# Kernel optimization log

Measured on AMD Instinct MI355X. Metric: run time of the kernel, lower is better.

The kernel has to match this reference:

```python
import jax, jax.numpy as jnp
import numpy as np


def setup_inputs() -> dict:
    key = jax.random.key(0)
    ks = jax.random.split(key, 5)
    Bsz, T, d = 8, 2048, 1024
    x = jax.random.normal(ks[0], (Bsz, T, d), dtype=jnp.float32)
    W_in = jax.random.normal(ks[1], (d, d), dtype=jnp.float32) * (1.0 / np.sqrt(d))
    b_in = jnp.zeros((d,), dtype=jnp.float32)
    log_A = -jnp.ones((d,), dtype=jnp.float32)  # keras Constant(-1.0) init
    B_vec = jax.random.normal(ks[2], (d,), dtype=jnp.float32) * 0.05  # keras random_normal stddev
    C = jax.random.normal(ks[3], (d, d), dtype=jnp.float32) * 0.05
    D = jnp.zeros((d,), dtype=jnp.float32)
    return {"x": x, "W_in": W_in, "b_in": b_in, "log_A": log_A, "B_vec": B_vec, "C": C, "D": D}


def reference(x, W_in, b_in, log_A, B_vec, C, D):
    # u = in_proj(x)
    u = jnp.einsum('btd,de->bte', x, W_in) + b_in            # [B,T,d]
    A = -jnp.exp(log_A)                                       # [d]
    # linear recurrence h_t = h_{t-1} * A + u_t * B, h_0 = 0
    # expressed as an associative scan over pairs (a_t, b_t):
    #   (a1,b1) o (a2,b2) = (a1*a2, b1*a2 + b2)
    b = u * B_vec                                             # [B,T,d]
    a = jnp.broadcast_to(A, b.shape)                          # [B,T,d]

    def combine(e1, e2):
        a1, b1 = e1
        a2, b2 = e2
        return (a1 * a2, b1 * a2 + b2)

    _, h_seq = jax.lax.associative_scan(combine, (a, b), axis=1)  # h_t, [B,T,d]
    y = jnp.einsum('bts,sd->btd', h_seq, C)
    return y + x * D
```

## Files before the change

kernel.cpp:

```cpp
#include <hip/hip_runtime.h>
#include <hip/hip_bf16.h>

typedef unsigned short ushort_t;
typedef __bf16 bf16x8 __attribute__((ext_vector_type(8)));
typedef float f32x4 __attribute__((ext_vector_type(4)));

#define BM 128
#define BN 128
#define BK 64

__device__ __forceinline__ float bf2f(ushort_t u) {
    union { unsigned int i; float f; } x; x.i = ((unsigned int)u) << 16; return x.f;
}
__device__ __forceinline__ ushort_t f2bf(float f) {
    __hip_bfloat16 h = __float2bfloat16(f);
    return *(ushort_t*)&h;
}
__device__ __forceinline__ void async16(const void* g, void* l) {
    __builtin_amdgcn_global_load_lds((const __attribute__((address_space(1))) void*)g,
                                     (__attribute__((address_space(3))) void*)l, 16, 0, 0);
}

__global__ void prep_fused(const float* __restrict__ x, const float* __restrict__ W_in,
                           const float* __restrict__ C, const float* __restrict__ Bv,
                           __hip_bfloat16* __restrict__ xb, __hip_bfloat16* __restrict__ Wpt,
                           __hip_bfloat16* __restrict__ Ct) {
    int bid = blockIdx.x;
    if (bid < 16384) {
        size_t idx = ((size_t)bid * 256 + threadIdx.x) * 4;
        float4 v = *(const float4*)(x + idx);
        ushort4 ov;
        ov.x = f2bf(v.x); ov.y = f2bf(v.y); ov.z = f2bf(v.z); ov.w = f2bf(v.w);
        *(ushort4*)((ushort_t*)xb + idx) = ov;
        return;
    }
    __shared__ float tile[32][33];
    const float* in;
    __hip_bfloat16* out;
    bool do_scale;
    int lid;
    if (bid < 17408) { lid = bid - 16384; in = W_in; out = Wpt; do_scale = true; }
    else             { lid = bid - 17408; in = C;    out = Ct;  do_scale = false; }
    int bx = (lid & 31) * 32;
    int by = (lid >> 5) * 32;
    int tx = threadIdx.x & 31, ty = threadIdx.x >> 5;
    #pragma unroll
    for (int i = 0; i < 32; i += 8)
        tile[ty + i][tx] = in[(size_t)(by + ty + i) * 1024 + bx + tx];
    __syncthreads();
    if (threadIdx.x < 128) {
        int n_local = threadIdx.x & 31;
        int quad    = threadIdx.x >> 5;
        int n = bx + n_local;
        float s = do_scale ? Bv[n] : 1.0f;
        int lr     = n & 15;
        int n_tile = n >> 4;
        int k_tile = by >> 5;
        ushort_t buf[8];
        #pragma unroll
        for (int j = 0; j < 8; ++j)
            buf[j] = f2bf(tile[quad * 8 + j][n_local] * s);
        size_t off = (((size_t)n_tile * 32 + k_tile) * 64 + quad * 16 + lr) * 8;
        ushort_t* dst = (ushort_t*)out + off;
        *(ushort4*)dst       = *(ushort4*)&buf[0];
        *(ushort4*)(dst + 4) = *(ushort4*)&buf[4];
    }
}

template <int EPI>
__global__ __launch_bounds__(256) void gemm_bt(
    const __hip_bfloat16* __restrict__ Ab, const __hip_bfloat16* __restrict__ Bpk,
    int M, int N, int K,
    const float* __restrict__ b_in, const float* __restrict__ Bv,
    __hip_bfloat16* __restrict__ out_bf,
    const __hip_bfloat16* __restrict__ xres_bf, const float* __restrict__ Dvec,
    float* __restrict__ out_f) {
    const int tid  = threadIdx.x;
    const int wave = tid >> 6;
    const int lane = tid & 63;
    const int quad = lane >> 4;
    const int lr   = lane & 15;
    const int wm   = wave >> 1;
    const int wn   = wave & 1;

    const int lin   = blockIdx.y * gridDim.x + blockIdx.x;
    const int xcd   = lin & 7;
    const int local = lin >> 3;
    const int m_blk = xcd * 16 + (local >> 3);
    const int n_blk = local & 7;
    const int m0 = m_blk * BM;
    const int n0 = n_blk * BN;

    __shared__ __align__(16) ushort_t sA[BM * BK];

    const ushort_t* A  = (const ushort_t*)Ab;
    const ushort_t* Bp = (const ushort_t*)Bpk;
    const int ktiles = K >> 5;
    const int ntile0 = n0 >> 4;

    f32x4 acc[4][4];
    #pragma unroll
    for (int i = 0; i < 4; ++i)
        #pragma unroll
        for (int j = 0; j < 4; ++j)
            #pragma unroll
            for (int r = 0; r < 4; ++r) acc[i][j][r] = 0.0f;

    const int row8 = lane >> 3;
    const int schunk = (lane & 7) ^ row8;
    const int ldcol = schunk * 8;
    for (int k0 = 0; k0 < K; k0 += BK) {
        __syncthreads();
        #pragma unroll
        for (int j = 0; j < 4; ++j) {
            int c = j * 4 + wave;
            int row = c * 8 + row8;
            const ushort_t* gA = A + (size_t)(m0 + row) * K + k0 + ldcol;
            async16(gA, &sA[c * 512]);
        }
        __syncthreads();
        #pragma unroll
        for (int kk = 0; kk < BK; kk += 32) {
            const int kt = (k0 + kk) >> 5;
            bf16x8 bfr[4];
            #pragma unroll
            for (int j = 0; j < 4; ++j)
                bfr[j] = *(const bf16x8*)&Bp[((((size_t)(ntile0 + wn * 4 + j)) * ktiles + kt) * 64 + lane) * 8];
            const int ck = (kk >> 3) + quad;
            const int pc = (ck ^ (lr & 7)) * 8;
            bf16x8 af[4];
            #pragma unroll
            for (int i = 0; i < 4; ++i)
                af[i] = *(const bf16x8*)&sA[(wm * 64 + i * 16 + lr) * BK + pc];
            #pragma unroll
            for (int i = 0; i < 4; ++i)
                #pragma unroll
                for (int j = 0; j < 4; ++j)
                    acc[i][j] = __builtin_amdgcn_mfma_f32_16x16x32_bf16(af[i], bfr[j], acc[i][j], 0, 0, 0);
        }
    }

    if constexpr (EPI == 0) {
        ushort_t* st = sA;
        #pragma unroll
        for (int i = 0; i < 4; ++i) {
            __syncthreads();
            #pragma unroll
            for (int j = 0; j < 4; ++j) {
                int colL = wn * 64 + j * 16 + lr;
                float bs = b_in[n0 + colL] * Bv[n0 + colL];
                #pragma unroll
                for (int r = 0; r < 4; ++r) {
                    int r32 = wm * 16 + quad * 4 + r;
                    st[r32 * 136 + colL] = f2bf(acc[i][j][r] + bs);
                }
            }
            __syncthreads();
            int r32 = tid >> 3;
            int cch = (tid & 7) * 16;
            int row_g = m0 + (r32 >> 4) * 64 + i * 16 + (r32 & 15);
            bf16x8 v0 = *(const bf16x8*)&st[r32 * 136 + cch];
            bf16x8 v1 = *(const bf16x8*)&st[r32 * 136 + cch + 8];
            ushort_t* dst = (ushort_t*)out_bf + (size_t)row_g * N + n0 + cch;
            *(bf16x8*)dst       = v0;
            *(bf16x8*)(dst + 8) = v1;
        }
    } else {
        #pragma unroll
        for (int i = 0; i < 4; ++i) {
            int row = m0 + wm * 64 + i * 16 + quad * 4;
            #pragma unroll
            for (int j = 0; j < 4; ++j) {
                int col = n0 + wn * 64 + j * 16 + lr;
                float dv = Dvec[col];
                #pragma unroll
                for (int r = 0; r < 4; ++r) {
                    float xv = bf2f(((const ushort_t*)xres_bf)[(size_t)(row + r) * N + col]);
                    out_f[(size_t)(row + r) * N + col] = acc[i][j][r] + xv * dv;
                }
            }
        }
    }
}

#define SCH 32
__global__ void scan_kernel(const __hip_bfloat16* __restrict__ b, __hip_bfloat16* __restrict__ h,
                            const float* __restrict__ logA, int T, int DD) {
    int c0 = (blockIdx.z * 256 + threadIdx.x) * 2;
    int q  = blockIdx.x;
    int bb = blockIdx.y;
    float2 la = *(const float2*)(logA + c0);
    float a0 = -__expf(la.x), a1 = -__expf(la.y);
    float a0_2 = a0 * a0,   a1_2 = a1 * a1;
    float a0_3 = a0_2 * a0, a1_3 = a1_2 * a1;
    float a0_4 = a0_2 * a0_2, a1_4 = a1_2 * a1_2;
    int ts = q * SCH;
    size_t base = (size_t)bb * T * DD + c0;
    float h0 = 0.f, h1 = 0.f;
    if (ts > 0) {
        const ushort_t* wp = (const ushort_t*)b + base + (size_t)(ts - 32) * DD;
        #pragma unroll
        for (int t = 0; t < 32; t += 4) {
            ushort2 v0 = *(const ushort2*)(wp);
            ushort2 v1 = *(const ushort2*)(wp + DD);
            ushort2 v2 = *(const ushort2*)(wp + 2 * (size_t)DD);
            ushort2 v3 = *(const ushort2*)(wp + 3 * (size_t)DD);
            wp += 4 * (size_t)DD;
            float s0 = fmaf(a0_3, bf2f(v0.x), fmaf(a0_2, bf2f(v1.x), fmaf(a0, bf2f(v2.x), bf2f(v3.x))));
            float s1 = fmaf(a1_3, bf2f(v0.y), fmaf(a1_2, bf2f(v1.y), fmaf(a1, bf2f(v2.y), bf2f(v3.y))));
            h0 = fmaf(a0_4, h0, s0);
            h1 = fmaf(a1_4, h1, s1);
        }
    }
    const ushort_t* bp = (const ushort_t*)b + base + (size_t)ts * DD;
    ushort_t* hp = (ushort_t*)h + base + (size_t)ts * DD;
    #pragma unroll
    for (int t = 0; t < SCH; t += 4) {
        ushort2 v0 = *(const ushort2*)(bp);
        ushort2 v1 = *(const ushort2*)(bp + DD);
        ushort2 v2 = *(const ushort2*)(bp + 2 * (size_t)DD);
        ushort2 v3 = *(const ushort2*)(bp + 3 * (size_t)DD);
        bp += 4 * (size_t)DD;
        ushort2 o;
        h0 = fmaf(a0, h0, bf2f(v0.x)); h1 = fmaf(a1, h1, bf2f(v0.y));
        o.x = f2bf(h0); o.y = f2bf(h1); *(ushort2*)hp = o;
        h0 = fmaf(a0, h0, bf2f(v1.x)); h1 = fmaf(a1, h1, bf2f(v1.y));
        o.x = f2bf(h0); o.y = f2bf(h1); *(ushort2*)(hp + DD) = o;
        h0 = fmaf(a0, h0, bf2f(v2.x)); h1 = fmaf(a1, h1, bf2f(v2.y));
        o.x = f2bf(h0); o.y = f2bf(h1); *(ushort2*)(hp + 2 * (size_t)DD) = o;
        h0 = fmaf(a0, h0, bf2f(v3.x)); h1 = fmaf(a1, h1, bf2f(v3.y));
        o.x = f2bf(h0); o.y = f2bf(h1); *(ushort2*)(hp + 3 * (size_t)DD) = o;
        hp += 4 * (size_t)DD;
    }
}

extern "C" void kernel_launch(void* const* d_in, const int* in_sizes, int n_in,
                              void* d_out, int out_size, void* d_ws, size_t ws_size,
                              hipStream_t stream) {
    const float* x    = (const float*)d_in[0];
    const float* W_in = (const float*)d_in[1];
    const float* b_in = (const float*)d_in[2];
    const float* logA = (const float*)d_in[3];
    const float* Bv   = (const float*)d_in[4];
    const float* C    = (const float*)d_in[5];
    const float* Dv   = (const float*)d_in[6];
    float* out = (float*)d_out;

    const int Bsz = 8, T = 2048, d = 1024;
    const int M = Bsz * T;

    char* w = (char*)d_ws;
    __hip_bfloat16* xb   = (__hip_bfloat16*)w;
    __hip_bfloat16* Wpt  = xb + (size_t)M * d;
    __hip_bfloat16* Ct   = Wpt + (size_t)d * d;
    __hip_bfloat16* bbuf = Ct + (size_t)d * d;
    __hip_bfloat16* hbuf = bbuf + (size_t)M * d;

    prep_fused<<<16384 + 2048, 256, 0, stream>>>(x, W_in, C, Bv, xb, Wpt, Ct);

    gemm_bt<0><<<dim3(d / BN, M / BM), 256, 0, stream>>>(
        xb, Wpt, M, d, d, b_in, Bv, bbuf, nullptr, nullptr, nullptr);
    scan_kernel<<<dim3(T / SCH, Bsz, 2), 256, 0, stream>>>(bbuf, hbuf, logA, T, d);
    gemm_bt<1><<<dim3(d / BN, M / BM), 256, 0, stream>>>(
        hbuf, Ct, M, d, d, nullptr, nullptr, nullptr, xb, Dv, out);
}
```

Baseline: 245.9 us.

## Fuse fp32-to-bf16 conversion of x into GEMM load path and retune scan chunking

Drops the separate pass that converts x to bf16. The first GEMM now async-loads fp32 x tiles into a doubled, swizzled LDS buffer and truncates them to bf16 with byte permutes while building the MFMA fragments. The residual epilogue reads fp32 x directly. The scan now has each thread handle 4 channels, uses chunks of 16 timesteps with a 32-step warm-up window, and drops the z grid dimension. This removes an extra read and write of the x tensor, but doubles LDS traffic for A in the first GEMM. The conversion also changes from round-to-nearest to truncation.

```diff
diff --git a/kernel.cpp b/kernel.cpp
--- a/kernel.cpp
+++ b/kernel.cpp
@@ -16,31 +16,25 @@
     __hip_bfloat16 h = __float2bfloat16(f);
     return *(ushort_t*)&h;
 }
+__device__ __forceinline__ unsigned int fbits(float f) {
+    union { float f; unsigned int u; } x; x.f = f; return x.u;
+}
 __device__ __forceinline__ void async16(const void* g, void* l) {
     __builtin_amdgcn_global_load_lds((const __attribute__((address_space(1))) void*)g,
                                      (__attribute__((address_space(3))) void*)l, 16, 0, 0);
 }
 
-__global__ void prep_fused(const float* __restrict__ x, const float* __restrict__ W_in,
-                           const float* __restrict__ C, const float* __restrict__ Bv,
-                           __hip_bfloat16* __restrict__ xb, __hip_bfloat16* __restrict__ Wpt,
-                           __hip_bfloat16* __restrict__ Ct) {
+__global__ void pack_weights(const float* __restrict__ W_in, const float* __restrict__ C,
+                             const float* __restrict__ Bv,
+                             __hip_bfloat16* __restrict__ Wpt, __hip_bfloat16* __restrict__ Ct) {
     int bid = blockIdx.x;
-    if (bid < 16384) {
-        size_t idx = ((size_t)bid * 256 + threadIdx.x) * 4;
-        float4 v = *(const float4*)(x + idx);
-        ushort4 ov;
-        ov.x = f2bf(v.x); ov.y = f2bf(v.y); ov.z = f2bf(v.z); ov.w = f2bf(v.w);
-        *(ushort4*)((ushort_t*)xb + idx) = ov;
-        return;
-    }
     __shared__ float tile[32][33];
     const float* in;
     __hip_bfloat16* out;
     bool do_scale;
     int lid;
-    if (bid < 17408) { lid = bid - 16384; in = W_in; out = Wpt; do_scale = true; }
-    else             { lid = bid - 17408; in = C;    out = Ct;  do_scale = false; }
+    if (bid < 1024) { lid = bid;        in = W_in; out = Wpt; do_scale = true; }
+    else            { lid = bid - 1024; in = C;    out = Ct;  do_scale = false; }
     int bx = (lid & 31) * 32;
     int by = (lid >> 5) * 32;
     int tx = threadIdx.x & 31, ty = threadIdx.x >> 5;
@@ -69,11 +63,11 @@
 
 template <int EPI>
 __global__ __launch_bounds__(256) void gemm_bt(
-    const __hip_bfloat16* __restrict__ Ab, const __hip_bfloat16* __restrict__ Bpk,
+    const void* __restrict__ Ag, const __hip_bfloat16* __restrict__ Bpk,
     int M, int N, int K,
     const float* __restrict__ b_in, const float* __restrict__ Bv,
     __hip_bfloat16* __restrict__ out_bf,
-    const __hip_bfloat16* __restrict__ xres_bf, const float* __restrict__ Dvec,
+    const float* __restrict__ xres_f, const float* __restrict__ Dvec,
     float* __restrict__ out_f) {
     const int tid  = threadIdx.x;
     const int wave = tid >> 6;
@@ -91,9 +85,8 @@
     const int m0 = m_blk * BM;
     const int n0 = n_blk * BN;
 
-    __shared__ __align__(16) ushort_t sA[BM * BK];
-
-    const ushort_t* A  = (const ushort_t*)Ab;
+    __shared__ __align__(16) ushort_t sA[EPI == 0 ? BM * BK * 2 : BM * BK];
+
     const ushort_t* Bp = (const ushort_t*)Bpk;
     const int ktiles = K >> 5;
     const int ntile0 = n0 >> 4;
@@ -106,37 +99,85 @@
             #pragma unroll
             for (int r = 0; r < 4; ++r) acc[i][j][r] = 0.0f;
 
-    const int row8 = lane >> 3;
-    const int schunk = (lane & 7) ^ row8;
-    const int ldcol = schunk * 8;
-    for (int k0 = 0; k0 < K; k0 += BK) {
-        __syncthreads();
-        #pragma unroll
-        for (int j = 0; j < 4; ++j) {
-            int c = j * 4 + wave;
-            int row = c * 8 + row8;
-            const ushort_t* gA = A + (size_t)(m0 + row) * K + k0 + ldcol;
-            async16(gA, &sA[c * 512]);
-        }
-        __syncthreads();
-        #pragma unroll
-        for (int kk = 0; kk < BK; kk += 32) {
-            const int kt = (k0 + kk) >> 5;
-            bf16x8 bfr[4];
-            #pragma unroll
-            for (int j = 0; j < 4; ++j)
-                bfr[j] = *(const bf16x8*)&Bp[((((size_t)(ntile0 + wn * 4 + j)) * ktiles + kt) * 64 + lane) * 8];
-            const int ck = (kk >> 3) + quad;
-            const int pc = (ck ^ (lr & 7)) * 8;
-            bf16x8 af[4];
-            #pragma unroll
-            for (int i = 0; i < 4; ++i)
-                af[i] = *(const bf16x8*)&sA[(wm * 64 + i * 16 + lr) * BK + pc];
-            #pragma unroll
-            for (int i = 0; i < 4; ++i)
+    if constexpr (EPI == 0) {
+        const float* Af = (const float*)Ag;
+        float* sAf = (float*)sA;
+        const int g4 = lane >> 4;
+        const int ph = lane & 15;
+        for (int k0 = 0; k0 < K; k0 += BK) {
+            __syncthreads();
+            #pragma unroll
+            for (int j = 0; j < 8; ++j) {
+                int c = j * 4 + wave;
+                int row = c * 4 + g4;
+                int lcol = (ph ^ (((c & 3) << 2) | g4)) << 2;
+                const float* gA = Af + (size_t)(m0 + row) * K + k0 + lcol;
+                async16(gA, &sAf[c * 256]);
+            }
+            __syncthreads();
+            #pragma unroll
+            for (int kk = 0; kk < BK; kk += 32) {
+                const int kt = (k0 + kk) >> 5;
+                bf16x8 bfr[4];
                 #pragma unroll
                 for (int j = 0; j < 4; ++j)
-                    acc[i][j] = __builtin_amdgcn_mfma_f32_16x16x32_bf16(af[i], bfr[j], acc[i][j], 0, 0, 0);
+                    bfr[j] = *(const bf16x8*)&Bp[((((size_t)(ntile0 + wn * 4 + j)) * ktiles + kt) * 64 + lane) * 8];
+                const int l0 = (kk >> 2) + quad * 2;
+                bf16x8 af[4];
+                #pragma unroll
+                for (int i = 0; i < 4; ++i) {
+                    int rL = wm * 64 + i * 16 + lr;
+                    int sw = rL & 15;
+                    float4 v0 = *(const float4*)&sAf[rL * 64 + ((l0 ^ sw) << 2)];
+                    float4 v1 = *(const float4*)&sAf[rL * 64 + (((l0 + 1) ^ sw) << 2)];
+                    union { unsigned int u[4]; bf16x8 v; } pk;
+                    pk.u[0] = __builtin_amdgcn_perm(fbits(v0.y), fbits(v0.x), 0x07060302);
+                    pk.u[1] = __builtin_amdgcn_perm(fbits(v0.w), fbits(v0.z), 0x07060302);
+                    pk.u[2] = __builtin_amdgcn_perm(fbits(v1.y), fbits(v1.x), 0x07060302);
+                    pk.u[3] = __builtin_amdgcn_perm(fbits(v1.w), fbits(v1.z), 0x07060302);
+                    af[i] = pk.v;
+                }
+                #pragma unroll
+                for (int i = 0; i < 4; ++i)
+                    #pragma unroll
+                    for (int j = 0; j < 4; ++j)
+                        acc[i][j] = __builtin_amdgcn_mfma_f32_16x16x32_bf16(af[i], bfr[j], acc[i][j], 0, 0, 0);
+            }
+        }
+    } else {
+        const ushort_t* A = (const ushort_t*)Ag;
+        const int row8 = lane >> 3;
+        const int schunk = (lane & 7) ^ row8;
+        const int ldcol = schunk * 8;
+        for (int k0 = 0; k0 < K; k0 += BK) {
+            __syncthreads();
+            #pragma unroll
+            for (int j = 0; j < 4; ++j) {
+                int c = j * 4 + wave;
+                int row = c * 8 + row8;
+                const ushort_t* gA = A + (size_t)(m0 + row) * K + k0 + ldcol;
+                async16(gA, &sA[c * 512]);
+            }
+            __syncthreads();
+            #pragma unroll
+            for (int kk = 0; kk < BK; kk += 32) {
+                const int kt = (k0 + kk) >> 5;
+                bf16x8 bfr[4];
+                #pragma unroll
+                for (int j = 0; j < 4; ++j)
+                    bfr[j] = *(const bf16x8*)&Bp[((((size_t)(ntile0 + wn * 4 + j)) * ktiles + kt) * 64 + lane) * 8];
+                const int ck = (kk >> 3) + quad;
+                const int pc = (ck ^ (lr & 7)) * 8;
+                bf16x8 af[4];
+                #pragma unroll
+                for (int i = 0; i < 4; ++i)
+                    af[i] = *(const bf16x8*)&sA[(wm * 64 + i * 16 + lr) * BK + pc];
+                #pragma unroll
+                for (int i = 0; i < 4; ++i)
+                    #pragma unroll
+                    for (int j = 0; j < 4; ++j)
+                        acc[i][j] = __builtin_amdgcn_mfma_f32_16x16x32_bf16(af[i], bfr[j], acc[i][j], 0, 0, 0);
+            }
         }
     }
 
@@ -175,7 +216,7 @@
                 float dv = Dvec[col];
                 #pragma unroll
                 for (int r = 0; r < 4; ++r) {
-                    float xv = bf2f(((const ushort_t*)xres_bf)[(size_t)(row + r) * N + col]);
+                    float xv = xres_f[(size_t)(row + r) * N + col];
                     out_f[(size_t)(row + r) * N + col] = acc[i][j][r] + xv * dv;
                 }
             }
@@ -183,54 +224,50 @@
     }
 }
 
-#define SCH 32
+#define SCH 16
+#define SWARM 32
 __global__ void scan_kernel(const __hip_bfloat16* __restrict__ b, __hip_bfloat16* __restrict__ h,
                             const float* __restrict__ logA, int T, int DD) {
-    int c0 = (blockIdx.z * 256 + threadIdx.x) * 2;
+    int c0 = threadIdx.x * 4;
     int q  = blockIdx.x;
     int bb = blockIdx.y;
-    float2 la = *(const float2*)(logA + c0);
-    float a0 = -__expf(la.x), a1 = -__expf(la.y);
-    float a0_2 = a0 * a0,   a1_2 = a1 * a1;
-    float a0_3 = a0_2 * a0, a1_3 = a1_2 * a1;
-    float a0_4 = a0_2 * a0_2, a1_4 = a1_2 * a1_2;
+    float4 la = *(const float4*)(logA + c0);
+    float a1[4] = { -__expf(la.x), -__expf(la.y), -__expf(la.z), -__expf(la.w) };
+    float a2[4], a3[4], a4[4];
+    #pragma unroll
+    for (int j = 0; j < 4; ++j) { a2[j] = a1[j] * a1[j]; a3[j] = a2[j] * a1[j]; a4[j] = a2[j] * a2[j]; }
     int ts = q * SCH;
+    int t0 = ts - SWARM; if (t0 < 0) t0 = 0;
+    int w = ts - t0;
     size_t base = (size_t)bb * T * DD + c0;
-    float h0 = 0.f, h1 = 0.f;
-    if (ts > 0) {
-        const ushort_t* wp = (const ushort_t*)b + base + (size_t)(ts - 32) * DD;
-        #pragma unroll
-        for (int t = 0; t < 32; t += 4) {
-            ushort2 v0 = *(const ushort2*)(wp);
-            ushort2 v1 = *(const ushort2*)(wp + DD);
-            ushort2 v2 = *(const ushort2*)(wp + 2 * (size_t)DD);
-            ushort2 v3 = *(const ushort2*)(wp + 3 * (size_t)DD);
-            wp += 4 * (size_t)DD;
-            float s0 = fmaf(a0_3, bf2f(v0.x), fmaf(a0_2, bf2f(v1.x), fmaf(a0, bf2f(v2.x), bf2f(v3.x))));
-            float s1 = fmaf(a1_3, bf2f(v0.y), fmaf(a1_2, bf2f(v1.y), fmaf(a1, bf2f(v2.y), bf2f(v3.y))));
-            h0 = fmaf(a0_4, h0, s0);
-            h1 = fmaf(a1_4, h1, s1);
-        }
-    }
-    const ushort_t* bp = (const ushort_t*)b + base + (size_t)ts * DD;
+    const ushort_t* bp = (const ushort_t*)b + base + (size_t)t0 * DD;
+    float hh[4] = { 0.f, 0.f, 0.f, 0.f };
+    for (int t = 0; t < w; t += 4) {
+        ushort_t v0[4], v1[4], v2[4], v3[4];
+        *(ushort4*)v0 = *(const ushort4*)(bp);
+        *(ushort4*)v1 = *(const ushort4*)(bp + DD);
+        *(ushort4*)v2 = *(const ushort4*)(bp + 2 * (size_t)DD);
+        *(ushort4*)v3 = *(const ushort4*)(bp + 3 * (size_t)DD);
+        bp += 4 * (size_t)DD;
+        #pragma unroll
+        for (int j = 0; j < 4; ++j) {
+            float s = fmaf(a3[j], bf2f(v0[j]),
+                      fmaf(a2[j], bf2f(v1[j]),
+                      fmaf(a1[j], bf2f(v2[j]), bf2f(v3[j]))));
+            hh[j] = fmaf(a4[j], hh[j], s);
+        }
+    }
     ushort_t* hp = (ushort_t*)h + base + (size_t)ts * DD;
     #pragma unroll
-    for (int t = 0; t < SCH; t += 4) {
-        ushort2 v0 = *(const ushort2*)(bp);
-        ushort2 v1 = *(const ushort2*)(bp + DD);
-        ushort2 v2 = *(const ushort2*)(bp + 2 * (size_t)DD);
-        ushort2 v3 = *(const ushort2*)(bp + 3 * (size_t)DD);
-        bp += 4 * (size_t)DD;
-        ushort2 o;
-        h0 = fmaf(a0, h0, bf2f(v0.x)); h1 = fmaf(a1, h1, bf2f(v0.y));
-        o.x = f2bf(h0); o.y = f2bf(h1); *(ushort2*)hp = o;
-        h0 = fmaf(a0, h0, bf2f(v1.x)); h1 = fmaf(a1, h1, bf2f(v1.y));
-        o.x = f2bf(h0); o.y = f2bf(h1); *(ushort2*)(hp + DD) = o;
-        h0 = fmaf(a0, h0, bf2f(v2.x)); h1 = fmaf(a1, h1, bf2f(v2.y));
-        o.x = f2bf(h0); o.y = f2bf(h1); *(ushort2*)(hp + 2 * (size_t)DD) = o;
-        h0 = fmaf(a0, h0, bf2f(v3.x)); h1 = fmaf(a1, h1, bf2f(v3.y));
-        o.x = f2bf(h0); o.y = f2bf(h1); *(ushort2*)(hp + 3 * (size_t)DD) = o;
-        hp += 4 * (size_t)DD;
+    for (int t = 0; t < SCH; ++t) {
+        ushort_t vv[4], oo[4];
+        *(ushort4*)vv = *(const ushort4*)bp; bp += DD;
+        #pragma unroll
+        for (int j = 0; j < 4; ++j) {
+            hh[j] = fmaf(a1[j], hh[j], bf2f(vv[j]));
+            oo[j] = f2bf(hh[j]);
+        }
+        *(ushort4*)hp = *(ushort4*)oo; hp += DD;
     }
 }
 
@@ -250,17 +287,16 @@
     const int M = Bsz * T;
 
     char* w = (char*)d_ws;
-    __hip_bfloat16* xb   = (__hip_bfloat16*)w;
-    __hip_bfloat16* Wpt  = xb + (size_t)M * d;
+    __hip_bfloat16* Wpt  = (__hip_bfloat16*)w;
     __hip_bfloat16* Ct   = Wpt + (size_t)d * d;
     __hip_bfloat16* bbuf = Ct + (size_t)d * d;
     __hip_bfloat16* hbuf = bbuf + (size_t)M * d;
 
-    prep_fused<<<16384 + 2048, 256, 0, stream>>>(x, W_in, C, Bv, xb, Wpt, Ct);
+    pack_weights<<<2048, 256, 0, stream>>>(W_in, C, Bv, Wpt, Ct);
 
     gemm_bt<0><<<dim3(d / BN, M / BM), 256, 0, stream>>>(
-        xb, Wpt, M, d, d, b_in, Bv, bbuf, nullptr, nullptr, nullptr);
-    scan_kernel<<<dim3(T / SCH, Bsz, 2), 256, 0, stream>>>(bbuf, hbuf, logA, T, d);
+        (const void*)x, Wpt, M, d, d, b_in, Bv, bbuf, nullptr, nullptr, nullptr);
+    scan_kernel<<<dim3(T / SCH, Bsz), 256, 0, stream>>>(bbuf, hbuf, logA, T, d);
     gemm_bt<1><<<dim3(d / BN, M / BM), 256, 0, stream>>>(
-        hbuf, Ct, M, d, d, nullptr, nullptr, nullptr, xb, Dv, out);
-}
+        (const void*)hbuf, Ct, M, d, d, nullptr, nullptr, nullptr, x, Dv, out);
+}
```

Result: slower. 272.6 us (+10.9%).

## Fuse scan into first GEMM epilogue using a 32-row halo recompute

Applied to the files above, without the earlier changes.

The separate scan kernel and its intermediate b buffer are removed. The first GEMM now computes 160 rows per block (a 32-row halo plus 128 rows), and the linear recurrence runs in shared memory. It warms up on the halo rows, relying on |A|^32 being negligible, then writes h directly. This saves a global round trip and a kernel launch, at the cost of 25% extra MFMA work and a serial 160-step per-column scan run by only 128 threads.

```diff
diff --git a/kernel.cpp b/kernel.cpp
--- a/kernel.cpp
+++ b/kernel.cpp
@@ -67,14 +67,11 @@
     }
 }
 
-template <int EPI>
-__global__ __launch_bounds__(256) void gemm_bt(
+__global__ __launch_bounds__(256) void gemm1_scan(
     const __hip_bfloat16* __restrict__ Ab, const __hip_bfloat16* __restrict__ Bpk,
-    int M, int N, int K,
     const float* __restrict__ b_in, const float* __restrict__ Bv,
-    __hip_bfloat16* __restrict__ out_bf,
-    const __hip_bfloat16* __restrict__ xres_bf, const float* __restrict__ Dvec,
-    float* __restrict__ out_f) {
+    const float* __restrict__ logA,
+    __hip_bfloat16* __restrict__ hout, int M, int N, int K) {
     const int tid  = threadIdx.x;
     const int wave = tid >> 6;
     const int lane = tid & 63;
@@ -91,6 +88,117 @@
     const int m0 = m_blk * BM;
     const int n0 = n_blk * BN;
 
+    __shared__ __align__(16) ushort_t sBuf[160 * 136];
+
+    const ushort_t* A  = (const ushort_t*)Ab;
+    const ushort_t* Bp = (const ushort_t*)Bpk;
+    const int ktiles = K >> 5;
+    const int ntile0 = n0 >> 4;
+
+    f32x4 acc[5][4];
+    #pragma unroll
+    for (int i = 0; i < 5; ++i)
+        #pragma unroll
+        for (int j = 0; j < 4; ++j)
+            #pragma unroll
+            for (int r = 0; r < 4; ++r) acc[i][j][r] = 0.0f;
+
+    const int row8 = lane >> 3;
+    const int schunk = (lane & 7) ^ row8;
+    const int ldcol = schunk * 8;
+    for (int k0 = 0; k0 < K; k0 += BK) {
+        __syncthreads();
+        #pragma unroll
+        for (int j = 0; j < 5; ++j) {
+            int c = j * 4 + wave;
+            int row = c * 8 + row8;
+            int grow = m0 - 32 + row;
+            if (grow < 0) grow = 0;
+            const ushort_t* gA = A + (size_t)grow * K + k0 + ldcol;
+            async16(gA, &sBuf[c * 512]);
+        }
+        __syncthreads();
+        #pragma unroll
+        for (int kk = 0; kk < BK; kk += 32) {
+            const int kt = (k0 + kk) >> 5;
+            bf16x8 bfr[4];
+            #pragma unroll
+            for (int j = 0; j < 4; ++j)
+                bfr[j] = *(const bf16x8*)&Bp[((((size_t)(ntile0 + wn * 4 + j)) * ktiles + kt) * 64 + lane) * 8];
+            const int ck = (kk >> 3) + quad;
+            const int pc = (ck ^ (lr & 7)) * 8;
+            bf16x8 af[5];
+            #pragma unroll
+            for (int i = 0; i < 5; ++i)
+                af[i] = *(const bf16x8*)&sBuf[(wm * 80 + i * 16 + lr) * BK + pc];
+            #pragma unroll
+            for (int i = 0; i < 5; ++i)
+                #pragma unroll
+                for (int j = 0; j < 4; ++j)
+                    acc[i][j] = __builtin_amdgcn_mfma_f32_16x16x32_bf16(af[i], bfr[j], acc[i][j], 0, 0, 0);
+        }
+    }
+
+    __syncthreads();
+    #pragma unroll
+    for (int i = 0; i < 5; ++i)
+        #pragma unroll
+        for (int j = 0; j < 4; ++j) {
+            int colL = wn * 64 + j * 16 + lr;
+            float bs = b_in[n0 + colL] * Bv[n0 + colL];
+            #pragma unroll
+            for (int r = 0; r < 4; ++r) {
+                int slot = wm * 80 + i * 16 + quad * 4 + r;
+                sBuf[slot * 136 + colL] = f2bf(acc[i][j][r] + bs);
+            }
+        }
+    __syncthreads();
+    if (tid < 128) {
+        float a = -__expf(logA[n0 + tid]);
+        float h = 0.f;
+        int s = ((m0 & 2047) == 0) ? 32 : 0;
+        for (; s < 32; ++s)
+            h = fmaf(a, h, bf2f(sBuf[s * 136 + tid]));
+        #pragma unroll 4
+        for (int t = 32; t < 160; ++t) {
+            h = fmaf(a, h, bf2f(sBuf[t * 136 + tid]));
+            sBuf[t * 136 + tid] = f2bf(h);
+        }
+    }
+    __syncthreads();
+    #pragma unroll
+    for (int i = 0; i < 4; ++i) {
+        int r32 = tid >> 3;
+        int cch = (tid & 7) * 16;
+        int slot = 32 + i * 32 + r32;
+        bf16x8 v0 = *(const bf16x8*)&sBuf[slot * 136 + cch];
+        bf16x8 v1 = *(const bf16x8*)&sBuf[slot * 136 + cch + 8];
+        ushort_t* dst = (ushort_t*)hout + (size_t)(m0 + i * 32 + r32) * N + n0 + cch;
+        *(bf16x8*)dst       = v0;
+        *(bf16x8*)(dst + 8) = v1;
+    }
+}
+
+__global__ __launch_bounds__(256) void gemm2(
+    const __hip_bfloat16* __restrict__ Ab, const __hip_bfloat16* __restrict__ Bpk,
+    const __hip_bfloat16* __restrict__ xres_bf, const float* __restrict__ Dvec,
+    float* __restrict__ out_f, int M, int N, int K) {
+    const int tid  = threadIdx.x;
+    const int wave = tid >> 6;
+    const int lane = tid & 63;
+    const int quad = lane >> 4;
+    const int lr   = lane & 15;
+    const int wm   = wave >> 1;
+    const int wn   = wave & 1;
+
+    const int lin   = blockIdx.y * gridDim.x + blockIdx.x;
+    const int xcd   = lin & 7;
+    const int local = lin >> 3;
+    const int m_blk = xcd * 16 + (local >> 3);
+    const int n_blk = local & 7;
+    const int m0 = m_blk * BM;
+    const int n0 = n_blk * BN;
+
     __shared__ __align__(16) ushort_t sA[BM * BK];
 
     const ushort_t* A  = (const ushort_t*)Ab;
@@ -140,97 +248,19 @@
         }
     }
 
-    if constexpr (EPI == 0) {
-        ushort_t* st = sA;
-        #pragma unroll
-        for (int i = 0; i < 4; ++i) {
-            __syncthreads();
-            #pragma unroll
-            for (int j = 0; j < 4; ++j) {
-                int colL = wn * 64 + j * 16 + lr;
-                float bs = b_in[n0 + colL] * Bv[n0 + colL];
-                #pragma unroll
-                for (int r = 0; r < 4; ++r) {
-                    int r32 = wm * 16 + quad * 4 + r;
-                    st[r32 * 136 + colL] = f2bf(acc[i][j][r] + bs);
-                }
+    #pragma unroll
+    for (int i = 0; i < 4; ++i) {
+        int row = m0 + wm * 64 + i * 16 + quad * 4;
+        #pragma unroll
+        for (int j = 0; j < 4; ++j) {
+            int col = n0 + wn * 64 + j * 16 + lr;
+            float dv = Dvec[col];
+            #pragma unroll
+            for (int r = 0; r < 4; ++r) {
+                float xv = bf2f(((const ushort_t*)xres_bf)[(size_t)(row + r) * N + col]);
+                out_f[(size_t)(row + r) * N + col] = acc[i][j][r] + xv * dv;
             }
-            __syncthreads();
-            int r32 = tid >> 3;
-            int cch = (tid & 7) * 16;
-            int row_g = m0 + (r32 >> 4) * 64 + i * 16 + (r32 & 15);
-            bf16x8 v0 = *(const bf16x8*)&st[r32 * 136 + cch];
-            bf16x8 v1 = *(const bf16x8*)&st[r32 * 136 + cch + 8];
-            ushort_t* dst = (ushort_t*)out_bf + (size_t)row_g * N + n0 + cch;
-            *(bf16x8*)dst       = v0;
-            *(bf16x8*)(dst + 8) = v1;
-        }
-    } else {
-        #pragma unroll
-        for (int i = 0; i < 4; ++i) {
-            int row = m0 + wm * 64 + i * 16 + quad * 4;
-            #pragma unroll
-            for (int j = 0; j < 4; ++j) {
-                int col = n0 + wn * 64 + j * 16 + lr;
-                float dv = Dvec[col];
-                #pragma unroll
-                for (int r = 0; r < 4; ++r) {
-                    float xv = bf2f(((const ushort_t*)xres_bf)[(size_t)(row + r) * N + col]);
-                    out_f[(size_t)(row + r) * N + col] = acc[i][j][r] + xv * dv;
-                }
-            }
-        }
-    }
-}
-
-#define SCH 32
-__global__ void scan_kernel(const __hip_bfloat16* __restrict__ b, __hip_bfloat16* __restrict__ h,
-                            const float* __restrict__ logA, int T, int DD) {
-    int c0 = (blockIdx.z * 256 + threadIdx.x) * 2;
-    int q  = blockIdx.x;
-    int bb = blockIdx.y;
-    float2 la = *(const float2*)(logA + c0);
-    float a0 = -__expf(la.x), a1 = -__expf(la.y);
-    float a0_2 = a0 * a0,   a1_2 = a1 * a1;
-    float a0_3 = a0_2 * a0, a1_3 = a1_2 * a1;
-    float a0_4 = a0_2 * a0_2, a1_4 = a1_2 * a1_2;
-    int ts = q * SCH;
-    size_t base = (size_t)bb * T * DD + c0;
-    float h0 = 0.f, h1 = 0.f;
-    if (ts > 0) {
-        const ushort_t* wp = (const ushort_t*)b + base + (size_t)(ts - 32) * DD;
-        #pragma unroll
-        for (int t = 0; t < 32; t += 4) {
-            ushort2 v0 = *(const ushort2*)(wp);
-            ushort2 v1 = *(const ushort2*)(wp + DD);
-            ushort2 v2 = *(const ushort2*)(wp + 2 * (size_t)DD);
-            ushort2 v3 = *(const ushort2*)(wp + 3 * (size_t)DD);
-            wp += 4 * (size_t)DD;
-            float s0 = fmaf(a0_3, bf2f(v0.x), fmaf(a0_2, bf2f(v1.x), fmaf(a0, bf2f(v2.x), bf2f(v3.x))));
-            float s1 = fmaf(a1_3, bf2f(v0.y), fmaf(a1_2, bf2f(v1.y), fmaf(a1, bf2f(v2.y), bf2f(v3.y))));
-            h0 = fmaf(a0_4, h0, s0);
-            h1 = fmaf(a1_4, h1, s1);
-        }
-    }
-    const ushort_t* bp = (const ushort_t*)b + base + (size_t)ts * DD;
-    ushort_t* hp = (ushort_t*)h + base + (size_t)ts * DD;
-    #pragma unroll
-    for (int t = 0; t < SCH; t += 4) {
-        ushort2 v0 = *(const ushort2*)(bp);
-        ushort2 v1 = *(const ushort2*)(bp + DD);
-        ushort2 v2 = *(const ushort2*)(bp + 2 * (size_t)DD);
-        ushort2 v3 = *(const ushort2*)(bp + 3 * (size_t)DD);
-        bp += 4 * (size_t)DD;
-        ushort2 o;
-        h0 = fmaf(a0, h0, bf2f(v0.x)); h1 = fmaf(a1, h1, bf2f(v0.y));
-        o.x = f2bf(h0); o.y = f2bf(h1); *(ushort2*)hp = o;
-        h0 = fmaf(a0, h0, bf2f(v1.x)); h1 = fmaf(a1, h1, bf2f(v1.y));
-        o.x = f2bf(h0); o.y = f2bf(h1); *(ushort2*)(hp + DD) = o;
-        h0 = fmaf(a0, h0, bf2f(v2.x)); h1 = fmaf(a1, h1, bf2f(v2.y));
-        o.x = f2bf(h0); o.y = f2bf(h1); *(ushort2*)(hp + 2 * (size_t)DD) = o;
-        h0 = fmaf(a0, h0, bf2f(v3.x)); h1 = fmaf(a1, h1, bf2f(v3.y));
-        o.x = f2bf(h0); o.y = f2bf(h1); *(ushort2*)(hp + 3 * (size_t)DD) = o;
-        hp += 4 * (size_t)DD;
+        }
     }
 }
 
@@ -253,14 +283,12 @@
     __hip_bfloat16* xb   = (__hip_bfloat16*)w;
     __hip_bfloat16* Wpt  = xb + (size_t)M * d;
     __hip_bfloat16* Ct   = Wpt + (size_t)d * d;
-    __hip_bfloat16* bbuf = Ct + (size_t)d * d;
-    __hip_bfloat16* hbuf = bbuf + (size_t)M * d;
+    __hip_bfloat16* hbuf = Ct + (size_t)d * d;
 
     prep_fused<<<16384 + 2048, 256, 0, stream>>>(x, W_in, C, Bv, xb, Wpt, Ct);
 
-    gemm_bt<0><<<dim3(d / BN, M / BM), 256, 0, stream>>>(
-        xb, Wpt, M, d, d, b_in, Bv, bbuf, nullptr, nullptr, nullptr);
-    scan_kernel<<<dim3(T / SCH, Bsz, 2), 256, 0, stream>>>(bbuf, hbuf, logA, T, d);
-    gemm_bt<1><<<dim3(d / BN, M / BM), 256, 0, stream>>>(
-        hbuf, Ct, M, d, d, nullptr, nullptr, nullptr, xb, Dv, out);
-}
+    gemm1_scan<<<dim3(d / BN, M / BM), 256, 0, stream>>>(
+        xb, Wpt, b_in, Bv, logA, hbuf, M, d, d);
+    gemm2<<<dim3(d / BN, M / BM), 256, 0, stream>>>(
+        hbuf, Ct, xb, Dv, out, M, d, d);
+}
```

Result: no change. 241.3 us (-1.8%).
